# Kernel tuning notes

Measured on AMD Instinct MI355X. Metric: run time of the kernel, lower is better.

The kernel has to match this reference:

```python
import jax, jax.numpy as jnp
import numpy as np

HID = 512
EMB = 345
SEQ = 512


def _lstm_dir(x, Wih, Whh, b, reverse):
    # x: (S, in), Wih: (4H, in), Whh: (4H, H), b: (4H,)  [torch gate order i,f,g,o]
    H = Whh.shape[1]
    zin = x @ Wih.T + b  # precompute input contribution: (S, 4H)

    def step(carry, z):
        h, c = carry
        z = z + h @ Whh.T
        i, f, g, o = jnp.split(z, 4)
        c = jax.nn.sigmoid(f) * c + jax.nn.sigmoid(i) * jnp.tanh(g)
        h = jax.nn.sigmoid(o) * jnp.tanh(c)
        return (h, c), h

    init = (jnp.zeros((H,), x.dtype), jnp.zeros((H,), x.dtype))
    _, hs = jax.lax.scan(step, init, zin, reverse=reverse)
    return hs  # (S, H), time-aligned for both directions


def _bilstm(x, Wih0, Whh0, b0, Wih_r, Whh_r, b_r):
    out = jnp.concatenate([
        _lstm_dir(x, Wih0[0], Whh0[0], b0[0], False),
        _lstm_dir(x, Wih0[1], Whh0[1], b0[1], True)], axis=-1)
    for l in range(Wih_r.shape[0]):  # remaining 3 stacked layers
        out = jnp.concatenate([
            _lstm_dir(out, Wih_r[l, 0], Whh_r[l, 0], b_r[l, 0], False),
            _lstm_dir(out, Wih_r[l, 1], Whh_r[l, 1], b_r[l, 1], True)], axis=-1)
    return out  # (S, 2H)


def setup_inputs() -> dict:
    key = jax.random.key(0)
    ks = jax.random.split(key, 16)
    H4, H2 = 4 * HID, 2 * HID
    s = 0.05
    x = jax.random.normal(ks[0], (SEQ, EMB), jnp.float32)
    heads = jax.random.randint(ks[1], (SEQ + 1,), 0, SEQ + 1)
    heads = heads.at[0].set(-1)  # root has no head
    Wih0 = jax.random.normal(ks[2], (2, H4, EMB), jnp.float32) * s
    Whh0 = jax.random.normal(ks[3], (2, H4, HID), jnp.float32) * s
    b0 = jax.random.normal(ks[4], (2, H4), jnp.float32) * s
    Wih_r = jax.random.normal(ks[5], (3, 2, H4, H2), jnp.float32) * s
    Whh_r = jax.random.normal(ks[6], (3, 2, H4, HID), jnp.float32) * s
    b_r = jax.random.normal(ks[7], (3, 2, H4), jnp.float32) * s
    W1 = jax.random.normal(ks[8], (256, 2 * H2), jnp.float32) * s
    b1 = jax.random.normal(ks[9], (256,), jnp.float32) * s
    W2 = jax.random.normal(ks[10], (128, 256), jnp.float32) * s
    b2 = jax.random.normal(ks[11], (128,), jnp.float32) * s
    W3 = jax.random.normal(ks[12], (64, 128), jnp.float32) * s
    b3 = jax.random.normal(ks[13], (64,), jnp.float32) * s
    W4 = jax.random.normal(ks[14], (1, 64), jnp.float32) * s
    b4 = jax.random.normal(ks[15], (1,), jnp.float32) * s
    return dict(x=x, heads=heads, Wih0=Wih0, Whh0=Whh0, b0=b0,
                Wih_r=Wih_r, Whh_r=Whh_r, b_r=b_r,
                W1=W1, b1=b1, W2=W2, b2=b2, W3=W3, b3=b3, W4=W4, b4=b4)


def reference(x, heads, Wih0, Whh0, b0, Wih_r, Whh_r, b_r,
              W1, b1, W2, b2, W3, b3, W4, b4):
    lstm_out = _bilstm(x, Wih0, Whh0, b0, Wih_r, Whh_r, b_r)  # (S, 2H)
    H2 = lstm_out.shape[-1]
    avail = jnp.concatenate([jnp.zeros((1, H2), x.dtype), lstm_out], axis=0)  # (N, 2H)
    N = avail.shape[0]
    # network(cat(w1, w2)) split: W1 acts on the two halves independently
    A = avail @ W1[:, :H2].T  # (N, 256)
    B = avail @ W1[:, H2:].T  # (N, 256)
    h1 = jax.nn.relu(A[:, None, :] + B[None, :, :] + b1)  # (N, N, 256)
    h2 = jax.nn.relu(h1 @ W2.T + b2)                       # (N, N, 128)
    h3 = jax.nn.relu(h2 @ W3.T + b3)                       # (N, N, 64)
    S = (h3 @ W4.T + b4)[..., 0]                           # (N, N) raw scores
    T = jnp.where(jnp.arange(N)[None, :] == heads[:, None], 100.0, 0.0)
    loss = jnp.sum((S - T) ** 2) / (N * N)  # sum of per-pair MSE / N^2
    probs = jax.nn.softmax(S, axis=1)  # scipy softmax(score_matrix, axis=1)
    return loss, probs
```

## Files before the change

kernel.cpp:

```cpp
#include <hip/hip_runtime.h>
#include <math.h>

#define HID 512
#define SEQ 512
#define EMB 345
#define NN  513
#define MPAD 576
#define H4  2048
#define H2  1024

__global__ __launch_bounds__(256)
void gemm_nt(const float* __restrict__ A, int lda, long aStride,
             const float* __restrict__ B, int ldb, long bStride,
             const float* __restrict__ bias, long biasStride,
             float* __restrict__ C, int ldc, long cStride, int K)
{
    int z = blockIdx.z;
    A += (long)z * aStride; B += (long)z * bStride; C += (long)z * cStride;
    const float* bptr = bias ? bias + (long)z * biasStride : nullptr;
    __shared__ float As[16][68];
    __shared__ float Bs[16][68];
    int tid = threadIdx.x;
    int tx = tid & 15, ty = tid >> 4;
    int m0 = blockIdx.y * 64, n0 = blockIdx.x * 64;
    float acc[4][4] = {};
    for (int k0 = 0; k0 < K; k0 += 16) {
        #pragma unroll
        for (int i = 0; i < 4; i++) {
            int id = tid + 256 * i;
            int mn = id >> 4, kk = id & 15;
            int k = k0 + kk;
            As[kk][mn] = (k < K) ? A[(long)(m0 + mn) * lda + k] : 0.f;
            Bs[kk][mn] = (k < K) ? B[(long)(n0 + mn) * ldb + k] : 0.f;
        }
        __syncthreads();
        #pragma unroll
        for (int kk = 0; kk < 16; kk++) {
            float a[4], b[4];
            #pragma unroll
            for (int i = 0; i < 4; i++) a[i] = As[kk][ty * 4 + i];
            #pragma unroll
            for (int j = 0; j < 4; j++) b[j] = Bs[kk][tx * 4 + j];
            #pragma unroll
            for (int i = 0; i < 4; i++)
                #pragma unroll
                for (int j = 0; j < 4; j++) acc[i][j] += a[i] * b[j];
        }
        __syncthreads();
    }
    #pragma unroll
    for (int i = 0; i < 4; i++) {
        int m = m0 + ty * 4 + i;
        #pragma unroll
        for (int j = 0; j < 4; j++) {
            int n = n0 + tx * 4 + j;
            float v = acc[i][j];
            if (bptr) v += bptr[n];
            C[(long)m * ldc + n] = v;
        }
    }
}

__device__ __forceinline__ float sigmf(float x)
{ return __builtin_amdgcn_rcpf(1.f + __expf(-x)); }
__device__ __forceinline__ float tanhf_fast(float x)
{ return 1.f - 2.f * __builtin_amdgcn_rcpf(1.f + __expf(2.f * x)); }

__global__ __launch_bounds__(256, 1)
void lstm_layer(const float* __restrict__ zin,
                const float* __restrict__ Whh,
                float* out)
{
    int wg  = blockIdx.x;
    int dir = wg >> 5;
    int kb  = (wg & 31) * 16;
    int tid = threadIdx.x;
    int lane = tid & 63;
    int p = tid >> 6;
    int gate = lane >> 4;
    int kq = lane & 15;
    long row = (long)gate * 512 + kb + kq;

    __shared__ float h_lds[512];
    __shared__ float part[2][256];

    float4 wreg[32];
    const float4* wp = (const float4*)(Whh + ((long)dir * H4 + row) * HID + p * 128);
    #pragma unroll
    for (int j = 0; j < 32; j++) wreg[j] = wp[j];

    const float* zin_d = zin + (long)dir * SEQ * H4;
    float c_st = 0.f;

    h_lds[p * 128 + lane] = 0.f;
    h_lds[p * 128 + 64 + lane] = 0.f;

    for (int t = 0; t < SEQ; t++) {
        int at = (dir == 0) ? t : (SEQ - 1 - t);
        float z0 = 0.f, z1 = 0.f, z2 = 0.f, z3 = 0.f;
        if (tid < 16) {
            const float* zp = zin_d + (long)at * H4 + kb + tid;
            z0 = zp[0]; z1 = zp[512]; z2 = zp[1024]; z3 = zp[1536];
        }
        if (t > 0) {
            int at_prev = (dir == 0) ? (t - 1) : (SEQ - t);
            const unsigned long long* src =
                (const unsigned long long*)(out + (long)at_prev * H2 + dir * HID + p * 128)
                + lane;
            unsigned long long a = __hip_atomic_load(src, __ATOMIC_RELAXED, __HIP_MEMORY_SCOPE_AGENT);
            while (((unsigned)a == 0xFFFFFFFFu) | ((unsigned)(a >> 32) == 0xFFFFFFFFu)) {
                __builtin_amdgcn_s_sleep(1);
                a = __hip_atomic_load(src, __ATOMIC_RELAXED, __HIP_MEMORY_SCOPE_AGENT);
            }
            union { unsigned long long u; float2 f; } cv;
            cv.u = a;
            *(float2*)&h_lds[p * 128 + lane * 2] = cv.f;
        }
        const float4* h4 = (const float4*)(h_lds + p * 128);
        float4 av = {0.f, 0.f, 0.f, 0.f};
        #pragma unroll
        for (int j = 0; j < 32; j++) {
            float4 w = wreg[j], h = h4[j];
            av.x += w.x * h.x; av.y += w.y * h.y;
            av.z += w.z * h.z; av.w += w.w * h.w;
        }
        part[t & 1][tid] = (av.x + av.y) + (av.z + av.w);
        __syncthreads();
        if (p == 0) {
            const float* pb = part[t & 1];
            float rs = pb[lane] + pb[lane + 64] + pb[lane + 128] + pb[lane + 192];
            float rf = __shfl(rs, (lane & 15) + 16);
            float rg = __shfl(rs, (lane & 15) + 32);
            float ro = __shfl(rs, (lane & 15) + 48);
            if (lane < 16) {
                float zi = z0 + rs;
                float zf = z1 + rf;
                float zg = z2 + rg;
                float zo = z3 + ro;
                float cc = sigmf(zf) * c_st + sigmf(zi) * tanhf_fast(zg);
                c_st = cc;
                float hh = sigmf(zo) * tanhf_fast(cc);
                __hip_atomic_store(out + (long)at * H2 + dir * HID + kb + lane, hh,
                                   __ATOMIC_RELAXED, __HIP_MEMORY_SCOPE_AGENT);
            }
        }
    }
}

__global__ __launch_bounds__(256)
void build_avail(const float* __restrict__ lstm_out, float* __restrict__ avail)
{
    long idx = (long)blockIdx.x * 256 + threadIdx.x;
    if (idx >= (long)MPAD * H2) return;
    int i = (int)(idx >> 10);
    int c = (int)(idx & 1023);
    float v = 0.f;
    if (i >= 1 && i <= SEQ) v = lstm_out[(long)(i - 1) * H2 + c];
    avail[idx] = v;
}

__global__ __launch_bounds__(256)
void transpose_w(const float* __restrict__ W, float* __restrict__ WT, int rows, int cols)
{
    int idx = blockIdx.x * 256 + threadIdx.x;
    if (idx >= rows * cols) return;
    int rr = idx / cols, cc = idx % cols;
    WT[cc * rows + rr] = W[idx];
}

#define STR1 257
#define STR2 129
__global__ __launch_bounds__(256)
void pair_kernel(const float* __restrict__ Abuf, const float* __restrict__ Bbuf,
                 const float* __restrict__ b1, const float* __restrict__ W2T,
                 const float* __restrict__ b2, const float* __restrict__ W3T,
                 const float* __restrict__ b3, const float* __restrict__ W4,
                 const float* __restrict__ b4, float* __restrict__ S)
{
    __shared__ float At[8 * STR1];
    __shared__ float Bt[8 * STR1];
    __shared__ float b1s[256];
    __shared__ float h2s[64 * STR2];
    __shared__ float spart[4 * 64];
    int tid = threadIdx.x;
    int i0 = blockIdx.y * 8, j0 = blockIdx.x * 8;
    {
        int rr = tid >> 5;
        int cbase = (tid & 31) * 8;
        #pragma unroll
        for (int u = 0; u < 8; u++) {
            At[rr * STR1 + cbase + u] = Abuf[(long)(i0 + rr) * 256 + cbase + u];
            Bt[rr * STR1 + cbase + u] = Bbuf[(long)(j0 + rr) * 256 + cbase + u];
        }
        b1s[tid] = b1[tid];
    }
    __syncthreads();
    int w = tid >> 6;
    int lane = tid & 63;
    int ii = lane >> 3, jj = lane & 7;
    #pragma unroll 1
    for (int blk = 0; blk < 4; blk++) {
        int c2b = __builtin_amdgcn_readfirstlane(w * 32 + blk * 8);
        float acc[8] = {};
        #pragma unroll 4
        for (int c1 = 0; c1 < 256; c1++) {
            float h1v = At[ii * STR1 + c1] + Bt[jj * STR1 + c1] + b1s[c1];
            h1v = fmaxf(h1v, 0.f);
            const float* wrow = W2T + c1 * 128 + c2b;
            #pragma unroll
            for (int u = 0; u < 8; u++) acc[u] += wrow[u] * h1v;
        }
        #pragma unroll
        for (int u = 0; u < 8; u++)
            h2s[lane * STR2 + c2b + u] = fmaxf(acc[u] + b2[c2b + u], 0.f);
    }
    __syncthreads();
    float sp = 0.f;
    #pragma unroll 1
    for (int blk = 0; blk < 2; blk++) {
        int c3b = __builtin_amdgcn_readfirstlane(w * 16 + blk * 8);
        float acc[8] = {};
        #pragma unroll 4
        for (int c2 = 0; c2 < 128; c2++) {
            float h2v = h2s[lane * STR2 + c2];
            const float* wrow = W3T + c2 * 64 + c3b;
            #pragma unroll
            for (int u = 0; u < 8; u++) acc[u] += wrow[u] * h2v;
        }
        #pragma unroll
        for (int u = 0; u < 8; u++) {
            float v = fmaxf(acc[u] + b3[c3b + u], 0.f);
            sp += W4[c3b + u] * v;
        }
    }
    spart[w * 64 + lane] = sp;
    __syncthreads();
    if (tid < 64) {
        float s = spart[tid] + spart[64 + tid] + spart[128 + tid] + spart[192 + tid] + b4[0];
        int i = i0 + (tid >> 3), j = j0 + (tid & 7);
        if (i < NN && j < NN) S[(long)i * NN + j] = s;
    }
}

__global__ __launch_bounds__(256)
void softmax_row(const float* __restrict__ S, const int* __restrict__ heads,
                 float* __restrict__ probs, float* __restrict__ rowloss)
{
    int i = blockIdx.x;
    int tid = threadIdx.x;
    __shared__ float red[256];
    __shared__ float srow[NN];
    const float* Si = S + (long)i * NN;
    float mx = -1e30f;
    for (int j = tid; j < NN; j += 256) { float v = Si[j]; srow[j] = v; mx = fmaxf(mx, v); }
    red[tid] = mx; __syncthreads();
    for (int s = 128; s > 0; s >>= 1) { if (tid < s) red[tid] = fmaxf(red[tid], red[tid + s]); __syncthreads(); }
    mx = red[0]; __syncthreads();
    float sum = 0.f, sq = 0.f;
    int hd = heads[i];
    for (int j = tid; j < NN; j += 256) {
        float v = srow[j];
        sum += __expf(v - mx);
        float t = (j == hd) ? 100.f : 0.f;
        float d = v - t; sq += d * d;
    }
    red[tid] = sum; __syncthreads();
    for (int s = 128; s > 0; s >>= 1) { if (tid < s) red[tid] += red[tid + s]; __syncthreads(); }
    sum = red[0]; __syncthreads();
    red[tid] = sq; __syncthreads();
    for (int s = 128; s > 0; s >>= 1) { if (tid < s) red[tid] += red[tid + s]; __syncthreads(); }
    if (tid == 0) rowloss[i] = red[0];
    float inv = 1.f / sum;
    for (int j = tid; j < NN; j += 256) probs[(long)i * NN + j] = __expf(srow[j] - mx) * inv;
}

__global__ __launch_bounds__(256)
void finish_loss(const float* __restrict__ rowloss, float* __restrict__ out0)
{
    __shared__ float red[256];
    int tid = threadIdx.x;
    float s = 0.f;
    for (int i = tid; i < NN; i += 256) s += rowloss[i];
    red[tid] = s; __syncthreads();
    for (int k = 128; k > 0; k >>= 1) { if (tid < k) red[tid] += red[tid + k]; __syncthreads(); }
    if (tid == 0) out0[0] = red[0] / ((float)NN * (float)NN);
}

extern "C" void kernel_launch(void* const* d_in, const int* in_sizes, int n_in,
                              void* d_out, int out_size, void* d_ws, size_t ws_size,
                              hipStream_t stream)
{
    const float* x     = (const float*)d_in[0];
    const int*   heads = (const int*)  d_in[1];
    const float* Wih0  = (const float*)d_in[2];
    const float* Whh0  = (const float*)d_in[3];
    const float* b0    = (const float*)d_in[4];
    const float* Wih_r = (const float*)d_in[5];
    const float* Whh_r = (const float*)d_in[6];
    const float* b_r   = (const float*)d_in[7];
    const float* W1    = (const float*)d_in[8];
    const float* b1    = (const float*)d_in[9];
    const float* W2    = (const float*)d_in[10];
    const float* b2    = (const float*)d_in[11];
    const float* W3    = (const float*)d_in[12];
    const float* b3    = (const float*)d_in[13];
    const float* W4    = (const float*)d_in[14];
    const float* b4    = (const float*)d_in[15];
    float* out = (float*)d_out;

    char* ws = (char*)d_ws;
    const size_t o_zin  = 0;
    const size_t o_outA = o_zin  + (size_t)2 * SEQ * H4 * 4 + 512;
    const size_t o_outB = o_outA + (size_t)SEQ * H2 * 4 + 512;
    const size_t o_avail= o_outB + (size_t)SEQ * H2 * 4 + 512;
    const size_t o_Abuf = o_avail+ (size_t)MPAD * H2 * 4 + 512;
    const size_t o_Bbuf = o_Abuf + (size_t)MPAD * 256 * 4 + 512;
    const size_t o_W2T  = o_Bbuf + (size_t)MPAD * 256 * 4 + 512;
    const size_t o_W3T  = o_W2T  + 256 * 128 * 4 + 512;
    const size_t o_S    = o_W3T  + 128 * 64 * 4 + 512;
    const size_t o_rl   = o_S    + (size_t)NN * NN * 4 + 512;

    float* zin   = (float*)(ws + o_zin);
    float* outA  = (float*)(ws + o_outA);
    float* outB  = (float*)(ws + o_outB);
    float* avail = (float*)(ws + o_avail);
    float* Abuf  = (float*)(ws + o_Abuf);
    float* Bbuf  = (float*)(ws + o_Bbuf);
    float* W2T   = (float*)(ws + o_W2T);
    float* W3T   = (float*)(ws + o_W3T);
    float* Sbuf  = (float*)(ws + o_S);
    float* rowl  = (float*)(ws + o_rl);

    const size_t outBytes = (size_t)SEQ * H2 * 4;

    gemm_nt<<<dim3(H4 / 64, SEQ / 64, 2), 256, 0, stream>>>(
        x, EMB, 0, Wih0, EMB, (long)H4 * EMB, b0, H4,
        zin, H4, (long)SEQ * H4, EMB);
    hipMemsetAsync(outA, 0xFF, outBytes, stream);
    lstm_layer<<<64, 256, 0, stream>>>(zin, Whh0, outA);

    float* bufs[2] = { outA, outB };
    for (int l = 1; l <= 3; l++) {
        const float* src = bufs[(l - 1) & 1];
        float* dst = bufs[l & 1];
        gemm_nt<<<dim3(H4 / 64, SEQ / 64, 2), 256, 0, stream>>>(
            src, H2, 0, Wih_r + (size_t)(l - 1) * 2 * H4 * H2, H2, (long)H4 * H2,
            b_r + (size_t)(l - 1) * 2 * H4, H4,
            zin, H4, (long)SEQ * H4, H2);
        hipMemsetAsync(dst, 0xFF, outBytes, stream);
        lstm_layer<<<64, 256, 0, stream>>>(
            zin, Whh_r + (size_t)(l - 1) * 2 * H4 * HID, dst);
    }
    float* lstm_final = bufs[3 & 1];

    build_avail<<<(MPAD * H2) / 256, 256, 0, stream>>>(lstm_final, avail);

    gemm_nt<<<dim3(256 / 64, MPAD / 64, 1), 256, 0, stream>>>(
        avail, H2, 0, W1, 2048, 0, nullptr, 0, Abuf, 256, 0, H2);
    gemm_nt<<<dim3(256 / 64, MPAD / 64, 1), 256, 0, stream>>>(
        avail, H2, 0, W1 + 1024, 2048, 0, nullptr, 0, Bbuf, 256, 0, H2);

    transpose_w<<<(128 * 256) / 256, 256, 0, stream>>>(W2, W2T, 128, 256);
    transpose_w<<<(64 * 128) / 256, 256, 0, stream>>>(W3, W3T, 64, 128);

    pair_kernel<<<dim3(65, 65), 256, 0, stream>>>(
        Abuf, Bbuf, b1, W2T, b2, W3T, b3, W4, b4, Sbuf);

    softmax_row<<<NN, 256, 0, stream>>>(Sbuf, heads, out + 1, rowl);
    finish_loss<<<1, 256, 0, stream>>>(rowl, out);
}
```

Baseline: 4.805 ms.

## Make each wavefront own whole LSTM cells to drop the per-step block barrier

```diff
diff --git a/kernel.cpp b/kernel.cpp
--- a/kernel.cpp
+++ b/kernel.cpp
@@ -66,6 +66,9 @@
 __device__ __forceinline__ float tanhf_fast(float x)
 { return 1.f - 2.f * __builtin_amdgcn_rcpf(1.f + __expf(2.f * x)); }
 
+__device__ __forceinline__ bool badw(unsigned long long a)
+{ return ((unsigned)a == 0xFFFFFFFFu) || ((unsigned)(a >> 32) == 0xFFFFFFFFu); }
+
 __global__ __launch_bounds__(256, 1)
 void lstm_layer(const float* __restrict__ zin,
                 const float* __restrict__ Whh,
@@ -75,74 +78,78 @@
     int dir = wg >> 5;
     int kb  = (wg & 31) * 16;
     int tid = threadIdx.x;
-    int lane = tid & 63;
-    int p = tid >> 6;
-    int gate = lane >> 4;
-    int kq = lane & 15;
-    long row = (long)gate * 512 + kb + kq;
-
-    __shared__ float h_lds[512];
-    __shared__ float part[2][256];
-
-    float4 wreg[32];
-    const float4* wp = (const float4*)(Whh + ((long)dir * H4 + row) * HID + p * 128);
+    int p   = tid >> 6;
+    int l   = tid & 63;
+    int g   = l >> 4;
+    int ci  = (l >> 2) & 3;
+    int kp  = l & 3;
+    int cell = kb + 4 * p + ci;
+    long row = (long)g * 512 + cell;
+
+    __shared__ float hshare[4][4 * 132];
+
+    float wreg[128];
+    {
+        const float4* wp = (const float4*)(Whh + ((long)dir * H4 + row) * HID + kp * 128);
+        #pragma unroll
+        for (int j = 0; j < 32; j++) {
+            float4 w = wp[j];
+            wreg[4*j+0] = w.x; wreg[4*j+1] = w.y; wreg[4*j+2] = w.z; wreg[4*j+3] = w.w;
+        }
+    }
     #pragma unroll
-    for (int j = 0; j < 32; j++) wreg[j] = wp[j];
+    for (int j = 0; j < 128; j++) asm volatile("" : "+v"(wreg[j]));
 
     const float* zin_d = zin + (long)dir * SEQ * H4;
+    float* myLds = hshare[p];
     float c_st = 0.f;
-
-    h_lds[p * 128 + lane] = 0.f;
-    h_lds[p * 128 + 64 + lane] = 0.f;
+    bool actlane = (l < 16) && ((l & 3) == 0);
 
     for (int t = 0; t < SEQ; t++) {
         int at = (dir == 0) ? t : (SEQ - 1 - t);
-        float z0 = 0.f, z1 = 0.f, z2 = 0.f, z3 = 0.f;
-        if (tid < 16) {
-            const float* zp = zin_d + (long)at * H4 + kb + tid;
-            z0 = zp[0]; z1 = zp[512]; z2 = zp[1024]; z3 = zp[1536];
-        }
+        float zv = 0.f;
+        if (kp == 0) zv = zin_d[(long)at * H4 + (long)g * 512 + cell];
+
+        float acc = 0.f;
         if (t > 0) {
             int at_prev = (dir == 0) ? (t - 1) : (SEQ - t);
             const unsigned long long* src =
-                (const unsigned long long*)(out + (long)at_prev * H2 + dir * HID + p * 128)
-                + lane;
-            unsigned long long a = __hip_atomic_load(src, __ATOMIC_RELAXED, __HIP_MEMORY_SCOPE_AGENT);
-            while (((unsigned)a == 0xFFFFFFFFu) | ((unsigned)(a >> 32) == 0xFFFFFFFFu)) {
+                (const unsigned long long*)(out + (long)at_prev * H2 + dir * HID) + l * 4;
+            unsigned long long a0, a1, a2, a3;
+            for (;;) {
+                a0 = __hip_atomic_load(src + 0, __ATOMIC_RELAXED, __HIP_MEMORY_SCOPE_AGENT);
+                a1 = __hip_atomic_load(src + 1, __ATOMIC_RELAXED, __HIP_MEMORY_SCOPE_AGENT);
+                a2 = __hip_atomic_load(src + 2, __ATOMIC_RELAXED, __HIP_MEMORY_SCOPE_AGENT);
+                a3 = __hip_atomic_load(src + 3, __ATOMIC_RELAXED, __HIP_MEMORY_SCOPE_AGENT);
+                if (!(badw(a0) | badw(a1) | badw(a2) | badw(a3))) break;
                 __builtin_amdgcn_s_sleep(1);
-                a = __hip_atomic_load(src, __ATOMIC_RELAXED, __HIP_MEMORY_SCOPE_AGENT);
             }
-            union { unsigned long long u; float2 f; } cv;
-            cv.u = a;
-            *(float2*)&h_lds[p * 128 + lane * 2] = cv.f;
-        }
-        const float4* h4 = (const float4*)(h_lds + p * 128);
-        float4 av = {0.f, 0.f, 0.f, 0.f};
-        #pragma unroll
-        for (int j = 0; j < 32; j++) {
-            float4 w = wreg[j], h = h4[j];
-            av.x += w.x * h.x; av.y += w.y * h.y;
-            av.z += w.z * h.z; av.w += w.w * h.w;
-        }
-        part[t & 1][tid] = (av.x + av.y) + (av.z + av.w);
-        __syncthreads();
-        if (p == 0) {
-            const float* pb = part[t & 1];
-            float rs = pb[lane] + pb[lane + 64] + pb[lane + 128] + pb[lane + 192];
-            float rf = __shfl(rs, (lane & 15) + 16);
-            float rg = __shfl(rs, (lane & 15) + 32);
-            float ro = __shfl(rs, (lane & 15) + 48);
-            if (lane < 16) {
-                float zi = z0 + rs;
-                float zf = z1 + rf;
-                float zg = z2 + rg;
-                float zo = z3 + ro;
-                float cc = sigmf(zf) * c_st + sigmf(zi) * tanhf_fast(zg);
-                c_st = cc;
-                float hh = sigmf(zo) * tanhf_fast(cc);
-                __hip_atomic_store(out + (long)at * H2 + dir * HID + kb + lane, hh,
-                                   __ATOMIC_RELAXED, __HIP_MEMORY_SCOPE_AGENT);
+            union { unsigned long long u; float2 f; } u0{a0}, u1{a1}, u2{a2}, u3{a3};
+            float4 v0 = {u0.f.x, u0.f.y, u1.f.x, u1.f.y};
+            float4 v1 = {u2.f.x, u2.f.y, u3.f.x, u3.f.y};
+            float* dst = myLds + (l >> 4) * 132 + (l & 15) * 8;
+            ((float4*)dst)[0] = v0;
+            ((float4*)dst)[1] = v1;
+            const float4* hc = (const float4*)(myLds + kp * 132);
+            #pragma unroll
+            for (int j = 0; j < 32; j++) {
+                float4 h = hc[j];
+                acc += wreg[4*j+0] * h.x + wreg[4*j+1] * h.y
+                     + wreg[4*j+2] * h.z + wreg[4*j+3] * h.w;
             }
+        }
+        acc += __shfl_xor(acc, 1);
+        acc += __shfl_xor(acc, 2);
+        float zsum = acc + zv;
+        float zf = __shfl(zsum, (l & 15) + 16);
+        float zg = __shfl(zsum, (l & 15) + 32);
+        float zo = __shfl(zsum, (l & 15) + 48);
+        if (actlane) {
+            float cc = sigmf(zf) * c_st + sigmf(zsum) * tanhf_fast(zg);
+            c_st = cc;
+            float hh = sigmf(zo) * tanhf_fast(cc);
+            __hip_atomic_store(out + (long)at * H2 + dir * HID + cell, hh,
+                               __ATOMIC_RELAXED, __HIP_MEMORY_SCOPE_AGENT);
         }
     }
 }
```

Result: slower. 7.628 ms (+58.8%).
